# Optimization experiments

Measured on AMD Instinct MI355X. Metric: run time of the kernel, lower is better.

## Reference

```python
import jax, jax.numpy as jnp
import numpy as np

B, L, D = 4, 2048, 2048
NUM_HEADS = 1          # residual q[:, :, 0, :] only broadcasts when num_heads == 1
DEPTH = D // NUM_HEADS
LN_EPS = 1e-6


def setup_inputs() -> dict:
    key = jax.random.key(0)
    ks = jax.random.split(key, 13)
    s = 0.02
    return {
        "q_in": jax.random.normal(ks[0], (B, L, D), jnp.float32),
        "k_in": jax.random.normal(ks[1], (B, L, D), jnp.float32),
        "v_in": jax.random.normal(ks[2], (B, L, D), jnp.float32),
        "wq_w": jax.random.normal(ks[3], (D, D), jnp.float32) * s,
        "wq_b": jnp.zeros((D,), jnp.float32),
        "wk_w": jax.random.normal(ks[4], (D, D), jnp.float32) * s,
        "wk_b": jnp.zeros((D,), jnp.float32),
        "wv_w": jax.random.normal(ks[5], (D, D), jnp.float32) * s,
        "wv_b": jnp.zeros((D,), jnp.float32),
        "wo_w": jax.random.normal(ks[6], (D, D), jnp.float32) * s,
        "wo_b": jnp.zeros((D,), jnp.float32),
        "ln_g": jnp.ones((D,), jnp.float32),
        "ln_b": jnp.zeros((D,), jnp.float32),
    }


def _split_heads(x):
    # [B, L, D] -> [B, H, L, depth]
    b, l, _ = x.shape
    return x.reshape(b, l, NUM_HEADS, DEPTH).transpose(0, 2, 1, 3)


def reference(q_in, k_in, v_in, wq_w, wq_b, wk_w, wk_b, wv_w, wv_b,
              wo_w, wo_b, ln_g, ln_b):
    q = _split_heads(q_in @ wq_w + wq_b)   # [B,H,L,dh]
    k = _split_heads(k_in @ wk_w + wk_b)
    v = _split_heads(v_in @ wv_w + wv_b)

    scale = 1.0 / jnp.sqrt(jnp.asarray(DEPTH, q.dtype))
    logits = jnp.einsum("bhqd,bhkd->bhqk", q, k) * scale
    attn = jax.nn.softmax(logits, axis=-1)                 # [B,H,Lq,Lk]
    ctx = jnp.einsum("bhqk,bhkd->bhqd", attn, v)           # [B,H,Lq,dh]

    concat = ctx.transpose(0, 2, 1, 3).reshape(B, L, D)    # [B,L,D]
    out = concat @ wo_w + wo_b                             # dropout inactive (inference)

    # faithful quirk of the original: residual adds split-q at position 0
    # q[:, :, 0, :] has shape [B, H, dh] == [B, 1, D] since H == 1
    resid = out + q[:, :, 0, :]

    mu = jnp.mean(resid, axis=-1, keepdims=True)
    var = jnp.mean(jnp.square(resid - mu), axis=-1, keepdims=True)
    y = (resid - mu) * jax.lax.rsqrt(var + LN_EPS) * ln_g + ln_b
    return y, attn
```

## Files before the change

### kernel.cpp

```cpp
#include <hip/hip_runtime.h>
#include <hip/hip_bf16.h>
#include <stdint.h>


typedef __bf16 bf16x8 __attribute__((ext_vector_type(8)));
typedef __bf16 bf16x4 __attribute__((ext_vector_type(4)));
typedef float  floatx4 __attribute__((ext_vector_type(4)));

constexpr int    kB = 4, kL = 2048, kD = 2048;
constexpr float  kScale = 0.022097086912079608f;
constexpr float  kEps   = 1e-6f;
constexpr size_t kNE = (size_t)kB * kL * kD;
constexpr size_t kNW = (size_t)kD * kD;
constexpr long   kSB = 4194304;

__device__ __forceinline__ void gll16(const void* g, void* l) {
    __builtin_amdgcn_global_load_lds(
        (__attribute__((address_space(1))) void*)(void*)g,
        (__attribute__((address_space(3))) void*)l, 16, 0, 0);
}

struct bfpair { __bf16 h, l; };
__device__ __forceinline__ bfpair split_bf16(float x) {
    bfpair p;
    p.h = (__bf16)x;
    p.l = (__bf16)(x - (float)p.h);
    return p;
}

template<bool CONVA, bool BIAS, bool WF32, bool WHL>
__global__ __launch_bounds__(256)
void gemm_hl(const float* __restrict__ Af,
             const __bf16* __restrict__ Ah, const __bf16* __restrict__ Al,
             const __bf16* __restrict__ Bh, const __bf16* __restrict__ Bl,
             const float* __restrict__ bias,
             float* __restrict__ Cf, __bf16* __restrict__ Ch, __bf16* __restrict__ Cl,
             int M, int N, int K, long sA, long sB, long sC, float scale)
{
    __shared__ __bf16 sAh[128 * 32], sAl[128 * 32];
    __shared__ __bf16 sBh[128 * 32], sBl[128 * 32];

    const int tid  = threadIdx.x;
    const int lane = tid & 63;
    const int wid  = tid >> 6;
    const int wr   = wid >> 1, wc = wid & 1;
    const int m0   = blockIdx.y * 128, n0 = blockIdx.x * 128;

    const size_t aoff = (size_t)blockIdx.z * sA;
    const size_t boff = (size_t)blockIdx.z * sB;
    const size_t coff = (size_t)blockIdx.z * sC;

    floatx4 acc[4][4];
#pragma unroll
    for (int m = 0; m < 4; ++m)
#pragma unroll
        for (int n = 0; n < 4; ++n) acc[m][n] = floatx4{0.f, 0.f, 0.f, 0.f};

    const int frow  = lane & 15;
    const int kblk  = lane >> 4;
    const int aBase = (wr * 64 + frow) * 32 + kblk * 8;
    const int bBase = (wc * 64 + frow) * 32 + kblk * 8;
    const int srow = lane >> 2;
    const int scol = (lane & 3) * 8;

    for (int kt = 0; kt < K; kt += 32) {
        if constexpr (CONVA) {
#pragma unroll
            for (int j = 0; j < 4; ++j) {
                int flat = j * 64 + lane;
                int r  = wid * 32 + (flat >> 3);
                int kq = (flat & 7) * 4;
                float4 v = *(const float4*)(Af + aoff + (size_t)(m0 + r) * K + kt + kq);
                bf16x4 hv, lv;
                bfpair p0 = split_bf16(v.x); hv[0] = p0.h; lv[0] = p0.l;
                bfpair p1 = split_bf16(v.y); hv[1] = p1.h; lv[1] = p1.l;
                bfpair p2 = split_bf16(v.z); hv[2] = p2.h; lv[2] = p2.l;
                bfpair p3 = split_bf16(v.w); hv[3] = p3.h; lv[3] = p3.l;
                *(bf16x4*)&sAh[r * 32 + kq] = hv;
                *(bf16x4*)&sAl[r * 32 + kq] = lv;
            }
        } else {
#pragma unroll
            for (int i = 0; i < 2; ++i) {
                int rb = wid * 32 + i * 16;
                gll16(Ah + aoff + (size_t)(m0 + rb + srow) * K + kt + scol, &sAh[rb * 32]);
                gll16(Al + aoff + (size_t)(m0 + rb + srow) * K + kt + scol, &sAl[rb * 32]);
            }
        }
#pragma unroll
        for (int i = 0; i < 2; ++i) {
            int rb = wid * 32 + i * 16;
            gll16(Bh + boff + (size_t)(n0 + rb + srow) * K + kt + scol, &sBh[rb * 32]);
            gll16(Bl + boff + (size_t)(n0 + rb + srow) * K + kt + scol, &sBl[rb * 32]);
        }
        __syncthreads();

        bf16x8 ah_[4], al_[4], bh_[4], bl_[4];
#pragma unroll
        for (int m = 0; m < 4; ++m) {
            ah_[m] = *(const bf16x8*)&sAh[aBase + m * 512];
            al_[m] = *(const bf16x8*)&sAl[aBase + m * 512];
        }
#pragma unroll
        for (int n = 0; n < 4; ++n) {
            bh_[n] = *(const bf16x8*)&sBh[bBase + n * 512];
            bl_[n] = *(const bf16x8*)&sBl[bBase + n * 512];
        }
#pragma unroll
        for (int m = 0; m < 4; ++m)
#pragma unroll
            for (int n = 0; n < 4; ++n) {
                acc[m][n] = __builtin_amdgcn_mfma_f32_16x16x32_bf16(ah_[m], bh_[n], acc[m][n], 0, 0, 0);
                acc[m][n] = __builtin_amdgcn_mfma_f32_16x16x32_bf16(ah_[m], bl_[n], acc[m][n], 0, 0, 0);
                acc[m][n] = __builtin_amdgcn_mfma_f32_16x16x32_bf16(al_[m], bh_[n], acc[m][n], 0, 0, 0);
            }
        __syncthreads();
    }

    const int crow0 = m0 + wr * 64 + ((lane >> 4) << 2);
    const int ccol0 = n0 + wc * 64 + (lane & 15);
#pragma unroll
    for (int n = 0; n < 4; ++n) {
        const int col = ccol0 + n * 16;
        const float bv = BIAS ? bias[col] : 0.f;
#pragma unroll
        for (int m = 0; m < 4; ++m)
#pragma unroll
            for (int j = 0; j < 4; ++j) {
                const size_t idx = coff + (size_t)(crow0 + m * 16 + j) * N + col;
                const float x = acc[m][n][j] * scale + bv;
                if constexpr (WF32) Cf[idx] = x;
                if constexpr (WHL) {
                    bfpair p = split_bf16(x);
                    Ch[idx] = p.h; Cl[idx] = p.l;
                }
            }
    }
}

__global__ __launch_bounds__(256)
void convert_wT(const float* __restrict__ w, __bf16* __restrict__ th, __bf16* __restrict__ tl)
{
    __shared__ float t[64][65];
    const int tid = threadIdx.x;
    const int r0 = blockIdx.y * 64, c0 = blockIdx.x * 64;
#pragma unroll
    for (int i = 0; i < 4; ++i) {
        int flat = i * 256 + tid;
        int r = flat >> 4, c4 = (flat & 15) * 4;
        float4 v = *(const float4*)(w + (size_t)(r0 + r) * kD + c0 + c4);
        t[r][c4 + 0] = v.x; t[r][c4 + 1] = v.y; t[r][c4 + 2] = v.z; t[r][c4 + 3] = v.w;
    }
    __syncthreads();
#pragma unroll
    for (int i = 0; i < 4; ++i) {
        int flat = i * 256 + tid;
        int c = flat >> 4, r4 = (flat & 15) * 4;
        bf16x4 hv, lv;
#pragma unroll
        for (int j = 0; j < 4; ++j) {
            bfpair p = split_bf16(t[r4 + j][c]);
            hv[j] = p.h; lv[j] = p.l;
        }
        *(bf16x4*)&th[(size_t)(c0 + c) * kD + r0 + r4] = hv;
        *(bf16x4*)&tl[(size_t)(c0 + c) * kD + r0 + r4] = lv;
    }
}

__global__ __launch_bounds__(256)
void transpose_hl(const __bf16* __restrict__ sh, const __bf16* __restrict__ sl,
                  __bf16* __restrict__ dh, __bf16* __restrict__ dl)
{
    __shared__ __bf16 t[64][73];
    const int b  = blockIdx.z >> 1;
    const bool lo = blockIdx.z & 1;
    const __bf16* src = (lo ? sl : sh) + (size_t)b * kSB;
    __bf16*       dst = (lo ? dl : dh) + (size_t)b * kSB;
    const int tid = threadIdx.x;
    const int r0 = blockIdx.y * 64, c0 = blockIdx.x * 64;
#pragma unroll
    for (int i = 0; i < 2; ++i) {
        int flat = i * 256 + tid;
        int r = flat >> 3, c8 = (flat & 7) * 8;
        bf16x8 v = *(const bf16x8*)&src[(size_t)(r0 + r) * kD + c0 + c8];
#pragma unroll
        for (int j = 0; j < 8; ++j) t[r][c8 + j] = v[j];
    }
    __syncthreads();
#pragma unroll
    for (int i = 0; i < 2; ++i) {
        int flat = i * 256 + tid;
        int c = flat >> 3, r8 = (flat & 7) * 8;
        bf16x8 v;
#pragma unroll
        for (int j = 0; j < 8; ++j) v[j] = t[r8 + j][c];
        *(bf16x8*)&dst[(size_t)(c0 + c) * kL + r0 + r8] = v;
    }
}

__global__ __launch_bounds__(256)
void softmax_rows(float* __restrict__ attn, __bf16* __restrict__ oh, __bf16* __restrict__ ol)
{
    const size_t base = (size_t)blockIdx.x * kL;
    const int tid = threadIdx.x, lane = tid & 63, wid = tid >> 6;

    float4 v0 = *(const float4*)(attn + base + tid * 8);
    float4 v1 = *(const float4*)(attn + base + tid * 8 + 4);
    float x[8] = {v0.x, v0.y, v0.z, v0.w, v1.x, v1.y, v1.z, v1.w};

    float m = x[0];
#pragma unroll
    for (int i = 1; i < 8; ++i) m = fmaxf(m, x[i]);
#pragma unroll
    for (int o = 32; o > 0; o >>= 1) m = fmaxf(m, __shfl_xor(m, o));

    __shared__ float rb[8];
    if (lane == 0) rb[wid] = m;
    __syncthreads();
    m = fmaxf(fmaxf(rb[0], rb[1]), fmaxf(rb[2], rb[3]));

    float s = 0.f;
#pragma unroll
    for (int i = 0; i < 8; ++i) { x[i] = __expf(x[i] - m); s += x[i]; }
#pragma unroll
    for (int o = 32; o > 0; o >>= 1) s += __shfl_xor(s, o);
    if (lane == 0) rb[4 + wid] = s;
    __syncthreads();
    s = rb[4] + rb[5] + rb[6] + rb[7];

    const float inv = 1.0f / s;
    bf16x8 hv, lv;
#pragma unroll
    for (int i = 0; i < 8; ++i) {
        x[i] *= inv;
        bfpair p = split_bf16(x[i]);
        hv[i] = p.h; lv[i] = p.l;
    }
    float4 o0 = {x[0], x[1], x[2], x[3]};
    float4 o1 = {x[4], x[5], x[6], x[7]};
    *(float4*)(attn + base + tid * 8)     = o0;
    *(float4*)(attn + base + tid * 8 + 4) = o1;
    *(bf16x8*)&oh[base + tid * 8] = hv;
    *(bf16x8*)&ol[base + tid * 8] = lv;
}

__global__ __launch_bounds__(256)
void copy_qrow0(const __bf16* __restrict__ qh, const __bf16* __restrict__ ql,
                float* __restrict__ q0)
{
    const int idx = blockIdx.x * 256 + threadIdx.x;
    const int b = idx >> 11, d = idx & 2047;
    const size_t off = (size_t)b * kSB + d;
    q0[idx] = (float)qh[off] + (float)ql[off];
}

__global__ __launch_bounds__(256)
void resid_ln(float* __restrict__ y, const float* __restrict__ q0,
              const float* __restrict__ g, const float* __restrict__ bet)
{
    const int row = blockIdx.x;
    const int b = row >> 11;
    const size_t ob = (size_t)row * kD;
    const int tid = threadIdx.x, lane = tid & 63, wid = tid >> 6;

    float4 a0 = *(const float4*)(y + ob + tid * 8);
    float4 a1 = *(const float4*)(y + ob + tid * 8 + 4);
    float4 q0v = *(const float4*)(q0 + b * 2048 + tid * 8);
    float4 q1v = *(const float4*)(q0 + b * 2048 + tid * 8 + 4);
    float x[8] = {a0.x + q0v.x, a0.y + q0v.y, a0.z + q0v.z, a0.w + q0v.w,
                  a1.x + q1v.x, a1.y + q1v.y, a1.z + q1v.z, a1.w + q1v.w};

    float s = 0.f, ss = 0.f;
#pragma unroll
    for (int i = 0; i < 8; ++i) { s += x[i]; ss += x[i] * x[i]; }
#pragma unroll
    for (int o = 32; o > 0; o >>= 1) { s += __shfl_xor(s, o); ss += __shfl_xor(ss, o); }
    __shared__ float rb[16];
    if (lane == 0) { rb[wid] = s; rb[8 + wid] = ss; }
    __syncthreads();
    s  = rb[0] + rb[1] + rb[2] + rb[3];
    ss = rb[8] + rb[9] + rb[10] + rb[11];

    const float mu  = s * (1.0f / kD);
    const float var = ss * (1.0f / kD) - mu * mu;
    const float rs  = rsqrtf(var + kEps);

    float4 g0 = *(const float4*)(g + tid * 8);
    float4 g1 = *(const float4*)(g + tid * 8 + 4);
    float4 b0 = *(const float4*)(bet + tid * 8);
    float4 b1 = *(const float4*)(bet + tid * 8 + 4);

    float4 o0, o1;
    o0.x = (x[0] - mu) * rs * g0.x + b0.x;
    o0.y = (x[1] - mu) * rs * g0.y + b0.y;
    o0.z = (x[2] - mu) * rs * g0.z + b0.z;
    o0.w = (x[3] - mu) * rs * g0.w + b0.w;
    o1.x = (x[4] - mu) * rs * g1.x + b1.x;
    o1.y = (x[5] - mu) * rs * g1.y + b1.y;
    o1.z = (x[6] - mu) * rs * g1.z + b1.z;
    o1.w = (x[7] - mu) * rs * g1.w + b1.w;
    *(float4*)(y + ob + tid * 8)     = o0;
    *(float4*)(y + ob + tid * 8 + 4) = o1;
}

extern "C" void kernel_launch(void* const* d_in, const int* in_sizes, int n_in,
                              void* d_out, int out_size, void* d_ws, size_t ws_size,
                              hipStream_t stream)
{
    (void)in_sizes; (void)n_in; (void)out_size; (void)ws_size;

    const float* q_in = (const float*)d_in[0];
    const float* k_in = (const float*)d_in[1];
    const float* v_in = (const float*)d_in[2];
    const float* wq_w = (const float*)d_in[3];
    const float* wq_b = (const float*)d_in[4];
    const float* wk_w = (const float*)d_in[5];
    const float* wk_b = (const float*)d_in[6];
    const float* wv_w = (const float*)d_in[7];
    const float* wv_b = (const float*)d_in[8];
    const float* wo_w = (const float*)d_in[9];
    const float* wo_b = (const float*)d_in[10];
    const float* ln_g = (const float*)d_in[11];
    const float* ln_b = (const float*)d_in[12];

    float* y    = (float*)d_out;
    float* attn = (float*)d_out + kNE;

    char* ws = (char*)d_ws;
    float*  qrow0 = (float*)ws;
    __bf16* slotA = (__bf16*)(ws + 32768);
    __bf16* slotB = slotA + 2 * kNE;
    __bf16* slotC = slotB + 2 * kNE;

    __bf16* wTh = (__bf16*)attn;
    __bf16* wTl = wTh + kNW;
    __bf16* wToh = slotA;
    __bf16* wTol = wToh + kNW;

    __bf16 *qh = slotA, *ql = slotA + kNE;
    __bf16 *kh = slotB, *kl = slotB + kNE;
    __bf16 *vh = slotC, *vl = slotC + kNE;
    __bf16 *ath = slotA, *atl = slotA + kNE;
    __bf16 *vTh = slotB, *vTl = slotB + kNE;
    __bf16 *cth = slotC, *ctl = slotC + kNE;

    const dim3 blk(256);
    const dim3 gW(32, 32);
    const dim3 gT(32, 32, 8);
    const dim3 gProj(16, 64);
    const dim3 gBat(16, 16, 4);

    convert_wT<<<gW, blk, 0, stream>>>(wq_w, wTh, wTl);
    gemm_hl<true, true, false, true><<<gProj, blk, 0, stream>>>(
        q_in, nullptr, nullptr, wTh, wTl, wq_b, nullptr, qh, ql,
        8192, 2048, 2048, 0, 0, 0, 1.0f);
    copy_qrow0<<<dim3(32), blk, 0, stream>>>(qh, ql, qrow0);

    convert_wT<<<gW, blk, 0, stream>>>(wk_w, wTh, wTl);
    gemm_hl<true, true, false, true><<<gProj, blk, 0, stream>>>(
        k_in, nullptr, nullptr, wTh, wTl, wk_b, nullptr, kh, kl,
        8192, 2048, 2048, 0, 0, 0, 1.0f);

    convert_wT<<<gW, blk, 0, stream>>>(wv_w, wTh, wTl);
    gemm_hl<true, true, false, true><<<gProj, blk, 0, stream>>>(
        v_in, nullptr, nullptr, wTh, wTl, wv_b, nullptr, vh, vl,
        8192, 2048, 2048, 0, 0, 0, 1.0f);

    gemm_hl<false, false, true, false><<<gBat, blk, 0, stream>>>(
        nullptr, qh, ql, kh, kl, nullptr, attn, nullptr, nullptr,
        2048, 2048, 2048, kSB, kSB, kSB, kScale);

    softmax_rows<<<dim3(kB * kL), blk, 0, stream>>>(attn, ath, atl);

    transpose_hl<<<gT, blk, 0, stream>>>(vh, vl, vTh, vTl);

    gemm_hl<false, false, false, true><<<gBat, blk, 0, stream>>>(
        nullptr, ath, atl, vTh, vTl, nullptr, nullptr, cth, ctl,
        2048, 2048, 2048, kSB, kSB, kSB, 1.0f);

    convert_wT<<<gW, blk, 0, stream>>>(wo_w, wToh, wTol);
    gemm_hl<false, true, true, false><<<gProj, blk, 0, stream>>>(
        nullptr, cth, ctl, wToh, wTol, wo_b, y, nullptr, nullptr,
        8192, 2048, 2048, 0, 0, 0, 1.0f);

    resid_ln<<<dim3(kB * kL), blk, 0, stream>>>(y, qrow0, ln_g, ln_b);
}
```

Measured before the change: 1.639 ms.

## Drop split-bf16 three-pass GEMMs for single-pass bf16 everywhere

Every GEMM, including the projections, the QK^T and PV batches and the output projection, now does a single bf16 MFMA per tile. Before, each one ran three passes (hi*hi, hi*lo, lo*hi) to emulate fp32. The low-part buffers, their loads and their conversion stores are removed throughout, which halves intermediate memory traffic and the LDS footprint. The residual row q[:,0,:] is now computed exactly in fp32 by a small separate kernel, because it no longer comes from the hi/lo projection output. Accuracy of attn and y drops to bf16-input precision, which risks failing tolerance.

```diff
diff --git a/kernel.cpp b/kernel.cpp
--- a/kernel.cpp
+++ b/kernel.cpp
@@ -28,7 +28,7 @@
     return p;
 }
 
-template<bool CONVA, bool BIAS, bool WF32, bool WHL>
+template<bool CONVA, bool BIAS, bool WF32, bool WH, bool WLO, bool T3>
 __global__ __launch_bounds__(256)
 void gemm_hl(const float* __restrict__ Af,
              const __bf16* __restrict__ Ah, const __bf16* __restrict__ Al,
@@ -37,8 +37,11 @@
              float* __restrict__ Cf, __bf16* __restrict__ Ch, __bf16* __restrict__ Cl,
              int M, int N, int K, long sA, long sB, long sC, float scale)
 {
-    __shared__ __bf16 sAh[128 * 32], sAl[128 * 32];
-    __shared__ __bf16 sBh[128 * 32], sBl[128 * 32];
+    __shared__ __bf16 smem[(T3 ? 4 : 2) * 128 * 32];
+    __bf16* sAh = smem;
+    __bf16* sBh = smem + 4096;
+    __bf16* sAl = T3 ? smem + 8192  : nullptr;
+    __bf16* sBl = T3 ? smem + 12288 : nullptr;
 
     const int tid  = threadIdx.x;
     const int lane = tid & 63;
@@ -71,48 +74,60 @@
                 int r  = wid * 32 + (flat >> 3);
                 int kq = (flat & 7) * 4;
                 float4 v = *(const float4*)(Af + aoff + (size_t)(m0 + r) * K + kt + kq);
-                bf16x4 hv, lv;
-                bfpair p0 = split_bf16(v.x); hv[0] = p0.h; lv[0] = p0.l;
-                bfpair p1 = split_bf16(v.y); hv[1] = p1.h; lv[1] = p1.l;
-                bfpair p2 = split_bf16(v.z); hv[2] = p2.h; lv[2] = p2.l;
-                bfpair p3 = split_bf16(v.w); hv[3] = p3.h; lv[3] = p3.l;
-                *(bf16x4*)&sAh[r * 32 + kq] = hv;
-                *(bf16x4*)&sAl[r * 32 + kq] = lv;
+                if constexpr (T3) {
+                    bf16x4 hv, lv;
+                    bfpair p0 = split_bf16(v.x); hv[0] = p0.h; lv[0] = p0.l;
+                    bfpair p1 = split_bf16(v.y); hv[1] = p1.h; lv[1] = p1.l;
+                    bfpair p2 = split_bf16(v.z); hv[2] = p2.h; lv[2] = p2.l;
+                    bfpair p3 = split_bf16(v.w); hv[3] = p3.h; lv[3] = p3.l;
+                    *(bf16x4*)&sAh[r * 32 + kq] = hv;
+                    *(bf16x4*)&sAl[r * 32 + kq] = lv;
+                } else {
+                    bf16x4 hv;
+                    hv[0] = (__bf16)v.x; hv[1] = (__bf16)v.y;
+                    hv[2] = (__bf16)v.z; hv[3] = (__bf16)v.w;
+                    *(bf16x4*)&sAh[r * 32 + kq] = hv;
+                }
             }
         } else {
 #pragma unroll
             for (int i = 0; i < 2; ++i) {
                 int rb = wid * 32 + i * 16;
                 gll16(Ah + aoff + (size_t)(m0 + rb + srow) * K + kt + scol, &sAh[rb * 32]);
-                gll16(Al + aoff + (size_t)(m0 + rb + srow) * K + kt + scol, &sAl[rb * 32]);
+                if constexpr (T3)
+                    gll16(Al + aoff + (size_t)(m0 + rb + srow) * K + kt + scol, &sAl[rb * 32]);
             }
         }
 #pragma unroll
         for (int i = 0; i < 2; ++i) {
             int rb = wid * 32 + i * 16;
             gll16(Bh + boff + (size_t)(n0 + rb + srow) * K + kt + scol, &sBh[rb * 32]);
-            gll16(Bl + boff + (size_t)(n0 + rb + srow) * K + kt + scol, &sBl[rb * 32]);
+            if constexpr (T3)
+                gll16(Bl + boff + (size_t)(n0 + rb + srow) * K + kt + scol, &sBl[rb * 32]);
         }
         __syncthreads();
 
-        bf16x8 ah_[4], al_[4], bh_[4], bl_[4];
+        bf16x8 ah_[4], bh_[4];
+        bf16x8 al_[4], bl_[4];
 #pragma unroll
         for (int m = 0; m < 4; ++m) {
             ah_[m] = *(const bf16x8*)&sAh[aBase + m * 512];
-            al_[m] = *(const bf16x8*)&sAl[aBase + m * 512];
+            if constexpr (T3) al_[m] = *(const bf16x8*)&sAl[aBase + m * 512];
         }
 #pragma unroll
         for (int n = 0; n < 4; ++n) {
             bh_[n] = *(const bf16x8*)&sBh[bBase + n * 512];
-            bl_[n] = *(const bf16x8*)&sBl[bBase + n * 512];
+            if constexpr (T3) bl_[n] = *(const bf16x8*)&sBl[bBase + n * 512];
         }
 #pragma unroll
         for (int m = 0; m < 4; ++m)
 #pragma unroll
             for (int n = 0; n < 4; ++n) {
                 acc[m][n] = __builtin_amdgcn_mfma_f32_16x16x32_bf16(ah_[m], bh_[n], acc[m][n], 0, 0, 0);
-                acc[m][n] = __builtin_amdgcn_mfma_f32_16x16x32_bf16(ah_[m], bl_[n], acc[m][n], 0, 0, 0);
-                acc[m][n] = __builtin_amdgcn_mfma_f32_16x16x32_bf16(al_[m], bh_[n], acc[m][n], 0, 0, 0);
+                if constexpr (T3) {
+                    acc[m][n] = __builtin_amdgcn_mfma_f32_16x16x32_bf16(ah_[m], bl_[n], acc[m][n], 0, 0, 0);
+                    acc[m][n] = __builtin_amdgcn_mfma_f32_16x16x32_bf16(al_[m], bh_[n], acc[m][n], 0, 0, 0);
+                }
             }
         __syncthreads();
     }
@@ -130,16 +145,20 @@
                 const size_t idx = coff + (size_t)(crow0 + m * 16 + j) * N + col;
                 const float x = acc[m][n][j] * scale + bv;
                 if constexpr (WF32) Cf[idx] = x;
-                if constexpr (WHL) {
-                    bfpair p = split_bf16(x);
-                    Ch[idx] = p.h; Cl[idx] = p.l;
+                if constexpr (WH) {
+                    if constexpr (WLO) {
+                        bfpair p = split_bf16(x);
+                        Ch[idx] = p.h; Cl[idx] = p.l;
+                    } else {
+                        Ch[idx] = (__bf16)x;
+                    }
                 }
             }
     }
 }
 
 __global__ __launch_bounds__(256)
-void convert_wT(const float* __restrict__ w, __bf16* __restrict__ th, __bf16* __restrict__ tl)
+void convert_wT(const float* __restrict__ w, __bf16* __restrict__ th)
 {
     __shared__ float t[64][65];
     const int tid = threadIdx.x;
@@ -156,33 +175,26 @@
     for (int i = 0; i < 4; ++i) {
         int flat = i * 256 + tid;
         int c = flat >> 4, r4 = (flat & 15) * 4;
-        bf16x4 hv, lv;
-#pragma unroll
-        for (int j = 0; j < 4; ++j) {
-            bfpair p = split_bf16(t[r4 + j][c]);
-            hv[j] = p.h; lv[j] = p.l;
-        }
+        bf16x4 hv;
+#pragma unroll
+        for (int j = 0; j < 4; ++j) hv[j] = (__bf16)t[r4 + j][c];
         *(bf16x4*)&th[(size_t)(c0 + c) * kD + r0 + r4] = hv;
-        *(bf16x4*)&tl[(size_t)(c0 + c) * kD + r0 + r4] = lv;
-    }
-}
-
-__global__ __launch_bounds__(256)
-void transpose_hl(const __bf16* __restrict__ sh, const __bf16* __restrict__ sl,
-                  __bf16* __restrict__ dh, __bf16* __restrict__ dl)
+    }
+}
+
+__global__ __launch_bounds__(256)
+void transpose_hl(const __bf16* __restrict__ src, __bf16* __restrict__ dst)
 {
     __shared__ __bf16 t[64][73];
-    const int b  = blockIdx.z >> 1;
-    const bool lo = blockIdx.z & 1;
-    const __bf16* src = (lo ? sl : sh) + (size_t)b * kSB;
-    __bf16*       dst = (lo ? dl : dh) + (size_t)b * kSB;
+    const __bf16* s = src + (size_t)blockIdx.z * kSB;
+    __bf16*       d = dst + (size_t)blockIdx.z * kSB;
     const int tid = threadIdx.x;
     const int r0 = blockIdx.y * 64, c0 = blockIdx.x * 64;
 #pragma unroll
     for (int i = 0; i < 2; ++i) {
         int flat = i * 256 + tid;
         int r = flat >> 3, c8 = (flat & 7) * 8;
-        bf16x8 v = *(const bf16x8*)&src[(size_t)(r0 + r) * kD + c0 + c8];
+        bf16x8 v = *(const bf16x8*)&s[(size_t)(r0 + r) * kD + c0 + c8];
 #pragma unroll
         for (int j = 0; j < 8; ++j) t[r][c8 + j] = v[j];
     }
@@ -194,12 +206,12 @@
         bf16x8 v;
 #pragma unroll
         for (int j = 0; j < 8; ++j) v[j] = t[r8 + j][c];
-        *(bf16x8*)&dst[(size_t)(c0 + c) * kL + r0 + r8] = v;
-    }
-}
-
-__global__ __launch_bounds__(256)
-void softmax_rows(float* __restrict__ attn, __bf16* __restrict__ oh, __bf16* __restrict__ ol)
+        *(bf16x8*)&d[(size_t)(c0 + c) * kL + r0 + r8] = v;
+    }
+}
+
+__global__ __launch_bounds__(256)
+void softmax_rows(float* __restrict__ attn, __bf16* __restrict__ oh)
 {
     const size_t base = (size_t)blockIdx.x * kL;
     const int tid = threadIdx.x, lane = tid & 63, wid = tid >> 6;
@@ -229,29 +241,34 @@
     s = rb[4] + rb[5] + rb[6] + rb[7];
 
     const float inv = 1.0f / s;
-    bf16x8 hv, lv;
+    bf16x8 hv;
 #pragma unroll
     for (int i = 0; i < 8; ++i) {
         x[i] *= inv;
-        bfpair p = split_bf16(x[i]);
-        hv[i] = p.h; lv[i] = p.l;
+        hv[i] = (__bf16)x[i];
     }
     float4 o0 = {x[0], x[1], x[2], x[3]};
     float4 o1 = {x[4], x[5], x[6], x[7]};
     *(float4*)(attn + base + tid * 8)     = o0;
     *(float4*)(attn + base + tid * 8 + 4) = o1;
     *(bf16x8*)&oh[base + tid * 8] = hv;
-    *(bf16x8*)&ol[base + tid * 8] = lv;
-}
-
-__global__ __launch_bounds__(256)
-void copy_qrow0(const __bf16* __restrict__ qh, const __bf16* __restrict__ ql,
-                float* __restrict__ q0)
+}
+
+__global__ __launch_bounds__(256)
+void qrow0_exact(const float* __restrict__ qin, const float* __restrict__ w,
+                 const float* __restrict__ bias, float* __restrict__ q0)
 {
     const int idx = blockIdx.x * 256 + threadIdx.x;
     const int b = idx >> 11, d = idx & 2047;
-    const size_t off = (size_t)b * kSB + d;
-    q0[idx] = (float)qh[off] + (float)ql[off];
+    const float* qr = qin + (size_t)b * kL * kD;
+    float a0 = 0.f, a1 = 0.f, a2 = 0.f, a3 = 0.f;
+    for (int k = 0; k < kD; k += 4) {
+        a0 = fmaf(qr[k + 0], w[(size_t)(k + 0) * kD + d], a0);
+        a1 = fmaf(qr[k + 1], w[(size_t)(k + 1) * kD + d], a1);
+        a2 = fmaf(qr[k + 2], w[(size_t)(k + 2) * kD + d], a2);
+        a3 = fmaf(qr[k + 3], w[(size_t)(k + 3) * kD + d], a3);
+    }
+    q0[idx] = ((a0 + a1) + (a2 + a3)) + bias[d];
 }
 
 __global__ __launch_bounds__(256)
@@ -329,58 +346,56 @@
     char* ws = (char*)d_ws;
     float*  qrow0 = (float*)ws;
     __bf16* slotA = (__bf16*)(ws + 32768);
-    __bf16* slotB = slotA + 2 * kNE;
-    __bf16* slotC = slotB + 2 * kNE;
-
-    __bf16* wTh = (__bf16*)attn;
-    __bf16* wTl = wTh + kNW;
+    __bf16* slotB = slotA + kNE;
+    __bf16* slotC = slotB + kNE;
+
+    __bf16* wTh  = (__bf16*)attn;
+    __bf16* qh   = slotA;
+    __bf16* kh   = slotB;
+    __bf16* vh   = slotC;
+    __bf16* ath  = slotA;
+    __bf16* vTh  = slotB;
+    __bf16* cth  = slotC;
     __bf16* wToh = slotA;
-    __bf16* wTol = wToh + kNW;
-
-    __bf16 *qh = slotA, *ql = slotA + kNE;
-    __bf16 *kh = slotB, *kl = slotB + kNE;
-    __bf16 *vh = slotC, *vl = slotC + kNE;
-    __bf16 *ath = slotA, *atl = slotA + kNE;
-    __bf16 *vTh = slotB, *vTl = slotB + kNE;
-    __bf16 *cth = slotC, *ctl = slotC + kNE;
 
     const dim3 blk(256);
     const dim3 gW(32, 32);
-    const dim3 gT(32, 32, 8);
+    const dim3 gT(32, 32, 4);
     const dim3 gProj(16, 64);
     const dim3 gBat(16, 16, 4);
 
-    convert_wT<<<gW, blk, 0, stream>>>(wq_w, wTh, wTl);
-    gemm_hl<true, true, false, true><<<gProj, blk, 0, stream>>>(
-        q_in, nullptr, nullptr, wTh, wTl, wq_b, nullptr, qh, ql,
+    qrow0_exact<<<dim3(32), blk, 0, stream>>>(q_in, wq_w, wq_b, qrow0);
+
+    convert_wT<<<gW, blk, 0, stream>>>(wq_w, wTh);
+    gemm_hl<true, true, false, true, false, false><<<gProj, blk, 0, stream>>>(
+        q_in, nullptr, nullptr, wTh, nullptr, wq_b, nullptr, qh, nullptr,
         8192, 2048, 2048, 0, 0, 0, 1.0f);
-    copy_qrow0<<<dim3(32), blk, 0, stream>>>(qh, ql, qrow0);
-
-    convert_wT<<<gW, blk, 0, stream>>>(wk_w, wTh, wTl);
-    gemm_hl<true, true, false, true><<<gProj, blk, 0, stream>>>(
-        k_in, nullptr, nullptr, wTh, wTl, wk_b, nullptr, kh, kl,
+
+    convert_wT<<<gW, blk, 0, stream>>>(wk_w, wTh);
+    gemm_hl<true, true, false, true, false, false><<<gProj, blk, 0, stream>>>(
+        k_in, nullptr, nullptr, wTh, nullptr, wk_b, nullptr, kh, nullptr,
         8192, 2048, 2048, 0, 0, 0, 1.0f);
 
-    convert_wT<<<gW, blk, 0, stream>>>(wv_w, wTh, wTl);
-    gemm_hl<true, true, false, true><<<gProj, blk, 0, stream>>>(
-        v_in, nullptr, nullptr, wTh, wTl, wv_b, nullptr, vh, vl,
+    convert_wT<<<gW, blk, 0, stream>>>(wv_w, wTh);
+    gemm_hl<true, true, false, true, false, false><<<gProj, blk, 0, stream>>>(
+        v_in, nullptr, nullptr, wTh, nullptr, wv_b, nullptr, vh, nullptr,
         8192, 2048, 2048, 0, 0, 0, 1.0f);
 
-    gemm_hl<false, false, true, false><<<gBat, blk, 0, stream>>>(
-        nullptr, qh, ql, kh, kl, nullptr, attn, nullptr, nullptr,
+    gemm_hl<false, false, true, false, false, false><<<gBat, blk, 0, stream>>>(
+        nullptr, qh, nullptr, kh, nullptr, nullptr, attn, nullptr, nullptr,
         2048, 2048, 2048, kSB, kSB, kSB, kScale);
 
-    softmax_rows<<<dim3(kB * kL), blk, 0, stream>>>(attn, ath, atl);
-
-    transpose_hl<<<gT, blk, 0, stream>>>(vh, vl, vTh, vTl);
-
-    gemm_hl<false, false, false, true><<<gBat, blk, 0, stream>>>(
-        nullptr, ath, atl, vTh, vTl, nullptr, nullptr, cth, ctl,
+    softmax_rows<<<dim3(kB * kL), blk, 0, stream>>>(attn, ath);
+
+    transpose_hl<<<gT, blk, 0, stream>>>(vh, vTh);
+
+    gemm_hl<false, false, false, true, false, false><<<gBat, blk, 0, stream>>>(
+        nullptr, ath, nullptr, vTh, nullptr, nullptr, nullptr, cth, nullptr,
         2048, 2048, 2048, kSB, kSB, kSB, 1.0f);
 
-    convert_wT<<<gW, blk, 0, stream>>>(wo_w, wToh, wTol);
-    gemm_hl<false, true, true, false><<<gProj, blk, 0, stream>>>(
-        nullptr, cth, ctl, wToh, wTol, wo_b, y, nullptr, nullptr,
+    convert_wT<<<gW, blk, 0, stream>>>(wo_w, wToh);
+    gemm_hl<false, true, true, false, false, false><<<gProj, blk, 0, stream>>>(
+        nullptr, cth, nullptr, wToh, nullptr, wo_b, y, nullptr, nullptr,
         8192, 2048, 2048, 0, 0, 0, 1.0f);
 
     resid_ln<<<dim3(kB * kL), blk, 0, stream>>>(y, qrow0, ln_g, ln_b);
```

New measurement: 1.353 ms. 1.21x faster.
